# Performance work log

Measured on AMD Instinct MI355X. Metric: run time of the kernel, lower is better.

Reference implementation:

```python
import jax, jax.numpy as jnp
import numpy as np

B, L, D = 4, 4096, 1024
N_HEADS = 16
HEAD_SIZE = D // N_HEADS  # 64


def setup_inputs() -> dict:
    key = jax.random.key(0)
    k_x, k_w, k_m = jax.random.split(key, 3)
    x = jax.random.normal(k_x, (B, L, D), dtype=jnp.float32)
    # nn.Linear(D, 3*head_size, bias=False): weight (3*hs, D); store transposed (D, 3*hs)
    W_qkv = jax.random.normal(k_w, (D, 3 * HEAD_SIZE), dtype=jnp.float32) * (D ** -0.5)
    attn_mask = jax.random.randint(k_m, (B, L), 0, 2).astype(jnp.bool_)
    return {"x": x, "attn_mask": attn_mask, "W_qkv": W_qkv}


def reference(x, attn_mask, W_qkv):
    # x: (B, L, D); W_qkv: (D, 3*hs); attn_mask: (B, L) True = attend
    qkv = x @ W_qkv                                # (B, L, 3*hs)
    q, k, v = jnp.split(qkv, 3, axis=-1)           # each (B, L, hs)
    scale = HEAD_SIZE ** -0.5
    scores = jnp.einsum('bqd,bkd->bqk', q, k) * scale   # (B, L, L)
    neg_inf = jnp.finfo(scores.dtype).min
    scores = jnp.where(attn_mask[:, None, :], scores, neg_inf)
    weights = jax.nn.softmax(scores, axis=-1)      # (B, L, L)
    out = jnp.einsum('bqk,bkd->bqd', weights, v)   # (B, L, hs)
    return out
```

## Files before the change

### kernel.cpp

```cpp
#include <hip/hip_runtime.h>

typedef __bf16 bf16_t;
typedef __bf16 bf16x8 __attribute__((ext_vector_type(8)));
typedef __bf16 bf16x4 __attribute__((ext_vector_type(4)));
typedef __bf16 bf16x2 __attribute__((ext_vector_type(2)));
typedef float  f32x4  __attribute__((ext_vector_type(4)));
typedef float  f32x16 __attribute__((ext_vector_type(16)));
struct uint4_t { unsigned x, y, z, w; };

#define B_  4
#define L_  4096
#define D_  1024
#define HS  64
#define NQ  192
#define SCL2E 0.1803368801111204f
#define MFMA16 __builtin_amdgcn_mfma_f32_16x16x32_bf16
#define MFMA32 __builtin_amdgcn_mfma_f32_32x32x16_bf16

static __device__ __forceinline__ unsigned pk_bf16(float a, float b) {
    union { bf16x2 v; unsigned u; } x;
    x.v[0] = (bf16_t)a; x.v[1] = (bf16_t)b;
    return x.u;
}
static __device__ __forceinline__ void swap32(unsigned& x, unsigned& y) {
    asm("v_permlane32_swap_b32 %0, %1" : "+v"(x), "+v"(y));
}

__global__ __launch_bounds__(256) void pack_w_kernel(const void* __restrict__ Win,
                                                     const unsigned char* __restrict__ mask,
                                                     const unsigned short* __restrict__ xw,
                                                     bf16_t* __restrict__ Wtp,
                                                     int* __restrict__ flags,
                                                     bf16_t* __restrict__ m01) {
    __shared__ int c1, c23, cbad;
    int tid = threadIdx.x;
    if (tid == 0) { c1 = 0; c23 = 0; cbad = 0; }
    __syncthreads();
    uint4_t m[4];
#pragma unroll
    for (int i = 0; i < 4; ++i)
        m[i] = *(const uint4_t*)(mask + tid * 16 + i * 4096);
    int a = 0, bc = 0;
#pragma unroll
    for (int i = 0; i < 4; ++i) {
        const unsigned* w = (const unsigned*)&m[i];
#pragma unroll
        for (int j = 0; j < 4; ++j) {
            if (w[j] & 0x0000ff00u) a++;
            if (w[j] & 0xffff0000u) bc++;
        }
    }
    uint4_t xm = *(const uint4_t*)(xw + tid * 8);
    int bad = 0;
    const unsigned* xwv = (const unsigned*)&xm;
#pragma unroll
    for (int j = 0; j < 4; ++j)
#pragma unroll
        for (int h = 0; h < 2; ++h) {
            unsigned s = (xwv[j] >> (16 * h)) & 0xFFFFu;
            unsigned e = (s >> 7) & 0xFF;
            if (e > 150 || (e < 90 && e != 0)) bad++;
        }
    if (a)   atomicAdd(&c1, a);
    if (bc)  atomicAdd(&c23, bc);
    if (bad) atomicAdd(&cbad, bad);
    __syncthreads();
    int f32 = (cbad >= 64) ? 1 : 0;
    int kind = (c1 > 0) ? 1 : ((c23 > 0) ? 2 : 0);
    if (blockIdx.x == 0 && tid == 0) {
        flags[0] = kind;
        flags[1] = f32;
    }

    int idx = blockIdx.x * 256 + tid;

    if (idx < B_ * L_) {
        bool mv;
        if (kind == 1)      mv = mask[idx] != 0;
        else if (kind == 2) mv = ((const float*)mask)[idx] != 0.0f;
        else                mv = ((const int*)mask)[idx] != 0;
        m01[idx] = (bf16_t)(mv ? 1.0f : 0.0f);
    }

    int lane = idx & 63;
    int t    = (idx >> 6) & 3;
    int kc   = (idx >> 8) & 31;
    int ct   = idx >> 13;
    int n  = ct * 64 + t * 16 + (lane & 15);
    int k0 = kc * 32 + (lane >> 4) * 8;
    bf16x8 v;
#pragma unroll
    for (int j = 0; j < 8; ++j) {
        if (f32) v[j] = (bf16_t)(((const float*)Win)[(k0 + j) * NQ + n]);
        else     v[j] = ((const bf16_t*)Win)[(k0 + j) * NQ + n];
    }
    *(bf16x8*)(Wtp + (size_t)idx * 8) = v;
}

__global__ __launch_bounds__(256, 2) void qkv_gemm_kernel(const void* __restrict__ xin,
                                                          const int* __restrict__ flags,
                                                          const bf16_t* __restrict__ Wtp,
                                                          const bf16_t* __restrict__ m01p,
                                                          bf16_t* __restrict__ Qb,
                                                          bf16_t* __restrict__ Kp,
                                                          bf16_t* __restrict__ Vp) {
    __shared__ __align__(16) bf16_t xs[32 * 520];
    __shared__ __align__(16) bf16_t sqk[32 * 136];
    __shared__ __align__(16) bf16_t sv[64 * 40];

    int tid = threadIdx.x;
    int wave = tid >> 6, lane = tid & 63, quad = lane >> 4, l16 = lane & 15;
    int rg = wave & 1, ch = wave >> 1;
    int m0 = blockIdx.x * 32;
    int xf = flags[1];

    f32x4 acc[6] = {};
    bf16x8 Ba[6], Bb[6];

    auto stage = [&](int h) {
        bf16x8 tmp[8];
#pragma unroll
        for (int j = 0; j < 8; ++j) {
            int c = tid + j * 256;
            int row = c >> 6, off = (c & 63) * 8;
            if (xf) {
                const float* xp = (const float*)xin + (size_t)(m0 + row) * D_ + h * 512 + off;
                f32x4 lo = *(const f32x4*)xp, hi = *(const f32x4*)(xp + 4);
                tmp[j][0] = (bf16_t)lo[0]; tmp[j][1] = (bf16_t)lo[1];
                tmp[j][2] = (bf16_t)lo[2]; tmp[j][3] = (bf16_t)lo[3];
                tmp[j][4] = (bf16_t)hi[0]; tmp[j][5] = (bf16_t)hi[1];
                tmp[j][6] = (bf16_t)hi[2]; tmp[j][7] = (bf16_t)hi[3];
            } else {
                tmp[j] = *(const bf16x8*)((const bf16_t*)xin + (size_t)(m0 + row) * D_ + h * 512 + off);
            }
        }
#pragma unroll
        for (int j = 0; j < 8; ++j) {
            int c = tid + j * 256;
            int row = c >> 6, off = (c & 63) * 8;
            *(bf16x8*)&xs[row * 520 + off] = tmp[j];
        }
    };
    auto loadB6 = [&](int ks, bf16x8* Bv) {
#pragma unroll
        for (int i = 0; i < 6; ++i) {
            int st = ch * 6 + i, ct2 = st >> 2, tt = st & 3;
            Bv[i] = *(const bf16x8*)(Wtp + ((size_t)(ct2 * 32 + ks) * 4 + tt) * 512 + lane * 8);
        }
    };
    auto compute6 = [&](int ks, const bf16x8* Bv) {
        bf16x8 A = *(const bf16x8*)&xs[(rg * 16 + l16) * 520 + (ks & 15) * 32 + quad * 8];
#pragma unroll
        for (int i = 0; i < 6; ++i)
            acc[i] = MFMA16(A, Bv[i], acc[i], 0, 0, 0);
    };

    stage(0);
    loadB6(0, Ba);
    __syncthreads();
#pragma unroll
    for (int half = 0; half < 2; ++half) {
        int base = half * 16;
        for (int m = 0; m < 16; m += 2) {
            int ks = base + m;
            loadB6(ks + 1, Bb);
            compute6(ks, Ba);
            loadB6(ks + 2 <= 31 ? ks + 2 : 31, Ba);
            compute6(ks + 1, Bb);
        }
        if (half == 0) {
            __syncthreads();
            stage(1);
            __syncthreads();
        }
    }

    int rowb = rg * 16 + quad * 4;
#pragma unroll
    for (int i = 0; i < 6; ++i) {
        int col = ch * 96 + i * 16 + l16;
#pragma unroll
        for (int r = 0; r < 4; ++r) {
            float av = acc[i][r];
            if (col < 64) av *= SCL2E;
            bf16_t hv = (bf16_t)av;
            if (col < 128) sqk[(rowb + r) * 136 + col] = hv;
            else           sv[(col - 128) * 40 + rowb + r] = hv;
        }
    }
    __syncthreads();

    int bb = m0 >> 12, l0 = m0 & 4095;
    int t64 = l0 >> 6, stile = (l0 >> 5) & 1, ctop = (l0 >> 4) & 2;
    {
        int row = tid >> 3, off = (tid & 7) * 8;
        bf16x8 v = *(const bf16x8*)&sqk[row * 136 + off];
        *(bf16x8*)(Qb + (size_t)(m0 + row) * HS + off) = v;
    }
    {
        int chk = tid >> 6, ln = tid & 63;
        bf16x8 v = *(const bf16x8*)&sqk[(tid & 31) * 136 + 64 + chk * 16 + ((tid >> 5) & 1) * 8];
        *(bf16x8*)(Kp + (size_t)bb * (L_ * HS) +
                   ((((size_t)t64 * 2 + stile) * 4 + chk) * 64 + ln) * 8) = v;
    }
    {
        int dt = tid >> 7, chL = (tid >> 6) & 1, ln = tid & 63;
        int hi2 = (tid >> 5) & 1, d31 = tid & 31;
        bf16x8 v  = *(const bf16x8*)&sv[(dt * 32 + d31) * 40 + chL * 16 + hi2 * 8];
        bf16x8 mm = *(const bf16x8*)(m01p + (size_t)m0 + chL * 16 + hi2 * 8);
        bf16x8 o;
#pragma unroll
        for (int j = 0; j < 8; ++j) o[j] = (bf16_t)((float)v[j] * (float)mm[j]);
        *(bf16x8*)(Vp + (size_t)bb * (L_ * HS) +
                   ((((size_t)t64 * 2 + dt) * 4 + ctop + chL) * 64 + ln) * 8) = o;
    }
}

template<int NSPLIT>
__global__ __launch_bounds__(256, 2) void attn_kernel(const bf16_t* __restrict__ Qb,
                                                      const bf16_t* __restrict__ Kp,
                                                      const bf16_t* __restrict__ Vp,
                                                      const bf16_t* __restrict__ m01p,
                                                      const int* __restrict__ flags,
                                                      float* __restrict__ Opart,
                                                      float* __restrict__ lpart,
                                                      void* __restrict__ outv) {
    constexpr int KCH = L_ / NSPLIT;
    constexpr int NHT = KCH / 32;

    int tid = threadIdx.x, wave = tid >> 6, lane = tid & 63;
    int hi = lane >> 5, l31 = lane & 31;
    int grp = blockIdx.x % (B_ * NSPLIT);
    int qt  = blockIdx.x / (B_ * NSPLIT);
    int sp = grp / B_, b = grp % B_;
    int q0 = qt * 128 + wave * 32;
    int hb = sp * NHT;

    const bf16_t* KpB = Kp + (size_t)b * (L_ * HS);
    const bf16_t* VpB = Vp + (size_t)b * (L_ * HS);
    const bf16_t* mB  = m01p + (size_t)b * L_ + sp * KCH;

    bf16x8 Qf[4];
    {
        const bf16_t* qp = Qb + (size_t)(b * L_ + q0 + l31) * HS + hi * 8;
#pragma unroll
        for (int c = 0; c < 4; ++c) Qf[c] = *(const bf16x8*)(qp + c * 16);
    }

    f32x16 O0 = {}, O1 = {}, den = {};

    auto loadK = [&](bf16x8* Kf, int t) {
        const bf16_t* kt = KpB + (size_t)(hb + t) * 2048;
#pragma unroll
        for (int c = 0; c < 4; ++c)
            Kf[c] = *(const bf16x8*)(kt + ((size_t)c * 64 + lane) * 8);
    };

    bf16x8 Kfr[4];
    loadK(Kfr, 0);

    for (int t = 0; t < NHT; ++t) {
        int ht = hb + t;
        int t64 = ht >> 1, stile = ht & 1;
        const bf16_t* vt = VpB + (size_t)t64 * 4096;
        const bf16_t* mt = mB + t * 32;

        bf16x8 V0[2], V1[2], Mf[2];
#pragma unroll
        for (int cc = 0; cc < 2; ++cc) {
            int chk = stile * 2 + cc;
            V0[cc] = *(const bf16x8*)(vt + (size_t)(0 * 4 + chk) * 512 + lane * 8);
            V1[cc] = *(const bf16x8*)(vt + (size_t)(1 * 4 + chk) * 512 + lane * 8);
            Mf[cc] = *(const bf16x8*)(mt + cc * 16 + hi * 8);
        }

        f32x16 S = {};
        __builtin_amdgcn_s_setprio(1);
#pragma unroll
        for (int c = 0; c < 4; ++c)
            S = MFMA32(Kfr[c], Qf[c], S, 0, 0, 0);
        __builtin_amdgcn_s_setprio(0);

        if (t + 1 < NHT) loadK(Kfr, t + 1);

#pragma unroll
        for (int r = 0; r < 16; ++r) S[r] = exp2f(S[r]);

#pragma unroll
        for (int cc = 0; cc < 2; ++cc) {
            unsigned w0 = pk_bf16(S[cc * 8 + 0], S[cc * 8 + 1]);
            unsigned w1 = pk_bf16(S[cc * 8 + 2], S[cc * 8 + 3]);
            unsigned w2 = pk_bf16(S[cc * 8 + 4], S[cc * 8 + 5]);
            unsigned w3 = pk_bf16(S[cc * 8 + 6], S[cc * 8 + 7]);
            swap32(w0, w2);
            swap32(w1, w3);
            union { unsigned u[4]; bf16x8 v; } P;
            P.u[0] = w0; P.u[1] = w1; P.u[2] = w2; P.u[3] = w3;
            __builtin_amdgcn_s_setprio(1);
            O0  = MFMA32(P.v, V0[cc], O0, 0, 0, 0);
            O1  = MFMA32(P.v, V1[cc], O1, 0, 0, 0);
            den = MFMA32(P.v, Mf[cc], den, 0, 0, 0);
            __builtin_amdgcn_s_setprio(0);
        }
    }

    if (NSPLIT == 1) {
        int of32 = flags[1];
#pragma unroll
        for (int r = 0; r < 16; ++r) {
            int qr = (r & 3) + 8 * (r >> 2) + 4 * hi;
            float inv = 1.0f / den[r];
            size_t base = (size_t)(b * L_ + q0 + qr) * HS;
            if (of32) {
                float* op = (float*)outv + base;
                op[l31]      = O0[r] * inv;
                op[32 + l31] = O1[r] * inv;
            } else {
                bf16_t* op = (bf16_t*)outv + base;
                op[l31]      = (bf16_t)(O0[r] * inv);
                op[32 + l31] = (bf16_t)(O1[r] * inv);
            }
        }
    } else {
        float* op = Opart + (size_t)sp * (B_ * L_ * HS) + (size_t)(b * L_ + q0) * HS + l31;
#pragma unroll
        for (int r = 0; r < 16; ++r) {
            int qr = (r & 3) + 8 * (r >> 2) + 4 * hi;
            op[(size_t)qr * HS]      = O0[r];
            op[(size_t)qr * HS + 32] = O1[r];
        }
        if (l31 == 0) {
            float* lp = lpart + (size_t)sp * (B_ * L_) + b * L_ + q0;
#pragma unroll
            for (int r = 0; r < 16; ++r)
                lp[(r & 3) + 8 * (r >> 2) + 4 * hi] = den[r];
        }
    }
}

__global__ __launch_bounds__(256) void reduce_kernel(const float* __restrict__ Opart,
                                                     const float* __restrict__ lpart,
                                                     const int* __restrict__ flags,
                                                     void* __restrict__ outv,
                                                     int nsplit) {
    int i4 = (blockIdx.x * 256 + threadIdx.x) * 4;
    int row = i4 >> 6;
    f32x4 acc = {};
    float lsum = 0.f;
    for (int s = 0; s < nsplit; ++s) {
        acc  += *(const f32x4*)&Opart[(size_t)s * (B_ * L_ * HS) + i4];
        lsum += lpart[(size_t)s * (B_ * L_) + row];
    }
    float inv = 1.0f / lsum;
    if (flags[1]) {
        f32x4 r = { acc[0] * inv, acc[1] * inv, acc[2] * inv, acc[3] * inv };
        *(f32x4*)&((float*)outv)[i4] = r;
    } else {
        bf16x4 r;
#pragma unroll
        for (int j = 0; j < 4; ++j) r[j] = (bf16_t)(acc[j] * inv);
        *(bf16x4*)&((bf16_t*)outv)[i4] = r;
    }
}

extern "C" void kernel_launch(void* const* d_in, const int* in_sizes, int n_in,
                              void* d_out, int out_size, void* d_ws, size_t ws_size,
                              hipStream_t stream) {
    (void)in_sizes; (void)n_in; (void)out_size;
    const void* x    = d_in[0];
    const void* mask = d_in[1];
    const void* W    = d_in[2];

    char* ws = (char*)d_ws;
    bf16_t* Qb    = (bf16_t*)(ws);
    bf16_t* Kp    = (bf16_t*)(ws + (2u << 20));
    bf16_t* Vp    = (bf16_t*)(ws + (4u << 20));
    bf16_t* Wtp   = (bf16_t*)(ws + (6u << 20));
    int*    flags = (int*)   (ws + (6u << 20) + (512u << 10));
    bf16_t* m01p  = (bf16_t*)(ws + (6u << 20) + (516u << 10));
    float*  Opart = (float*) (ws + (7u << 20));

    auto need = [](int ns) -> size_t {
        return (7u << 20) + (size_t)ns * (B_ * L_ * HS * 4)
                          + (size_t)ns * (B_ * L_ * 4) + 4096;
    };
    int nsplit = (ws_size >= need(8)) ? 8 : (ws_size >= need(4)) ? 4 : 1;
    float* lpart = (float*)(ws + (7u << 20) + (size_t)nsplit * (B_ * L_ * HS * 4));

    pack_w_kernel<<<96, 256, 0, stream>>>(W, (const unsigned char*)mask,
                                          (const unsigned short*)x, Wtp, flags, m01p);
    qkv_gemm_kernel<<<512, 256, 0, stream>>>(x, flags, Wtp, m01p, Qb, Kp, Vp);
    if (nsplit == 8) {
        attn_kernel<8><<<32 * B_ * 8, 256, 0, stream>>>(Qb, Kp, Vp, m01p, flags,
                                                        Opart, lpart, d_out);
        reduce_kernel<<<(B_ * L_ * HS) / 1024, 256, 0, stream>>>(Opart, lpart, flags,
                                                                 d_out, 8);
    } else if (nsplit == 4) {
        attn_kernel<4><<<32 * B_ * 4, 256, 0, stream>>>(Qb, Kp, Vp, m01p, flags,
                                                        Opart, lpart, d_out);
        reduce_kernel<<<(B_ * L_ * HS) / 1024, 256, 0, stream>>>(Opart, lpart, flags,
                                                                 d_out, 4);
    } else {
        attn_kernel<1><<<32 * B_, 256, 0, stream>>>(Qb, Kp, Vp, m01p, flags,
                                                    Opart, lpart, d_out);
    }
}
```

Measured before the change: 155.3 us.

## Process two 32-row query tiles per wave to reuse K/V/mask fragments

Each wave now handles 64 query rows, as two 32-row sub-tiles, instead of 32. The K, V and mask fragments loaded per key tile feed both sub-tiles, which halves global K/V traffic per query and halves the grid size. The cost is doubled accumulator registers, which could hurt occupancy under launch_bounds(256,2). The grid also shrinks (nsplit=8 gives 512 blocks), which reduces parallelism.

```diff
diff --git a/kernel.cpp b/kernel.cpp
--- a/kernel.cpp
+++ b/kernel.cpp
@@ -233,21 +233,26 @@
     int grp = blockIdx.x % (B_ * NSPLIT);
     int qt  = blockIdx.x / (B_ * NSPLIT);
     int sp = grp / B_, b = grp % B_;
-    int q0 = qt * 128 + wave * 32;
+    int q0 = qt * 256 + wave * 64;
     int hb = sp * NHT;
 
     const bf16_t* KpB = Kp + (size_t)b * (L_ * HS);
     const bf16_t* VpB = Vp + (size_t)b * (L_ * HS);
     const bf16_t* mB  = m01p + (size_t)b * L_ + sp * KCH;
 
-    bf16x8 Qf[4];
+    bf16x8 QfA[4], QfB[4];
     {
-        const bf16_t* qp = Qb + (size_t)(b * L_ + q0 + l31) * HS + hi * 8;
-#pragma unroll
-        for (int c = 0; c < 4; ++c) Qf[c] = *(const bf16x8*)(qp + c * 16);
-    }
-
-    f32x16 O0 = {}, O1 = {}, den = {};
+        const bf16_t* qa = Qb + (size_t)(b * L_ + q0 + l31) * HS + hi * 8;
+        const bf16_t* qb = Qb + (size_t)(b * L_ + q0 + 32 + l31) * HS + hi * 8;
+#pragma unroll
+        for (int c = 0; c < 4; ++c) {
+            QfA[c] = *(const bf16x8*)(qa + c * 16);
+            QfB[c] = *(const bf16x8*)(qb + c * 16);
+        }
+    }
+
+    f32x16 O0A = {}, O1A = {}, denA = {};
+    f32x16 O0B = {}, O1B = {}, denB = {};
 
     auto loadK = [&](bf16x8* Kf, int t) {
         const bf16_t* kt = KpB + (size_t)(hb + t) * 2048;
@@ -274,66 +279,105 @@
             Mf[cc] = *(const bf16x8*)(mt + cc * 16 + hi * 8);
         }
 
-        f32x16 S = {};
-        __builtin_amdgcn_s_setprio(1);
-#pragma unroll
-        for (int c = 0; c < 4; ++c)
-            S = MFMA32(Kfr[c], Qf[c], S, 0, 0, 0);
-        __builtin_amdgcn_s_setprio(0);
-
-        if (t + 1 < NHT) loadK(Kfr, t + 1);
-
-#pragma unroll
-        for (int r = 0; r < 16; ++r) S[r] = exp2f(S[r]);
-
-#pragma unroll
-        for (int cc = 0; cc < 2; ++cc) {
-            unsigned w0 = pk_bf16(S[cc * 8 + 0], S[cc * 8 + 1]);
-            unsigned w1 = pk_bf16(S[cc * 8 + 2], S[cc * 8 + 3]);
-            unsigned w2 = pk_bf16(S[cc * 8 + 4], S[cc * 8 + 5]);
-            unsigned w3 = pk_bf16(S[cc * 8 + 6], S[cc * 8 + 7]);
-            swap32(w0, w2);
-            swap32(w1, w3);
-            union { unsigned u[4]; bf16x8 v; } P;
-            P.u[0] = w0; P.u[1] = w1; P.u[2] = w2; P.u[3] = w3;
+        {
+            f32x16 S = {};
             __builtin_amdgcn_s_setprio(1);
-            O0  = MFMA32(P.v, V0[cc], O0, 0, 0, 0);
-            O1  = MFMA32(P.v, V1[cc], O1, 0, 0, 0);
-            den = MFMA32(P.v, Mf[cc], den, 0, 0, 0);
+#pragma unroll
+            for (int c = 0; c < 4; ++c)
+                S = MFMA32(Kfr[c], QfA[c], S, 0, 0, 0);
             __builtin_amdgcn_s_setprio(0);
+#pragma unroll
+            for (int r = 0; r < 16; ++r) S[r] = exp2f(S[r]);
+#pragma unroll
+            for (int cc = 0; cc < 2; ++cc) {
+                unsigned w0 = pk_bf16(S[cc * 8 + 0], S[cc * 8 + 1]);
+                unsigned w1 = pk_bf16(S[cc * 8 + 2], S[cc * 8 + 3]);
+                unsigned w2 = pk_bf16(S[cc * 8 + 4], S[cc * 8 + 5]);
+                unsigned w3 = pk_bf16(S[cc * 8 + 6], S[cc * 8 + 7]);
+                swap32(w0, w2);
+                swap32(w1, w3);
+                union { unsigned u[4]; bf16x8 v; } P;
+                P.u[0] = w0; P.u[1] = w1; P.u[2] = w2; P.u[3] = w3;
+                __builtin_amdgcn_s_setprio(1);
+                O0A  = MFMA32(P.v, V0[cc], O0A, 0, 0, 0);
+                O1A  = MFMA32(P.v, V1[cc], O1A, 0, 0, 0);
+                denA = MFMA32(P.v, Mf[cc], denA, 0, 0, 0);
+                __builtin_amdgcn_s_setprio(0);
+            }
+        }
+
+        {
+            f32x16 S = {};
+            __builtin_amdgcn_s_setprio(1);
+#pragma unroll
+            for (int c = 0; c < 4; ++c)
+                S = MFMA32(Kfr[c], QfB[c], S, 0, 0, 0);
+            __builtin_amdgcn_s_setprio(0);
+            if (t + 1 < NHT) loadK(Kfr, t + 1);
+#pragma unroll
+            for (int r = 0; r < 16; ++r) S[r] = exp2f(S[r]);
+#pragma unroll
+            for (int cc = 0; cc < 2; ++cc) {
+                unsigned w0 = pk_bf16(S[cc * 8 + 0], S[cc * 8 + 1]);
+                unsigned w1 = pk_bf16(S[cc * 8 + 2], S[cc * 8 + 3]);
+                unsigned w2 = pk_bf16(S[cc * 8 + 4], S[cc * 8 + 5]);
+                unsigned w3 = pk_bf16(S[cc * 8 + 6], S[cc * 8 + 7]);
+                swap32(w0, w2);
+                swap32(w1, w3);
+                union { unsigned u[4]; bf16x8 v; } P;
+                P.u[0] = w0; P.u[1] = w1; P.u[2] = w2; P.u[3] = w3;
+                __builtin_amdgcn_s_setprio(1);
+                O0B  = MFMA32(P.v, V0[cc], O0B, 0, 0, 0);
+                O1B  = MFMA32(P.v, V1[cc], O1B, 0, 0, 0);
+                denB = MFMA32(P.v, Mf[cc], denB, 0, 0, 0);
+                __builtin_amdgcn_s_setprio(0);
+            }
         }
     }
 
     if (NSPLIT == 1) {
         int of32 = flags[1];
 #pragma unroll
-        for (int r = 0; r < 16; ++r) {
-            int qr = (r & 3) + 8 * (r >> 2) + 4 * hi;
-            float inv = 1.0f / den[r];
-            size_t base = (size_t)(b * L_ + q0 + qr) * HS;
-            if (of32) {
-                float* op = (float*)outv + base;
-                op[l31]      = O0[r] * inv;
-                op[32 + l31] = O1[r] * inv;
-            } else {
-                bf16_t* op = (bf16_t*)outv + base;
-                op[l31]      = (bf16_t)(O0[r] * inv);
-                op[32 + l31] = (bf16_t)(O1[r] * inv);
+        for (int g = 0; g < 2; ++g) {
+            const f32x16& O0 = g ? O0B : O0A;
+            const f32x16& O1 = g ? O1B : O1A;
+            const f32x16& dn = g ? denB : denA;
+#pragma unroll
+            for (int r = 0; r < 16; ++r) {
+                int qr = (r & 3) + 8 * (r >> 2) + 4 * hi;
+                float inv = 1.0f / dn[r];
+                size_t base = (size_t)(b * L_ + q0 + g * 32 + qr) * HS;
+                if (of32) {
+                    float* op = (float*)outv + base;
+                    op[l31]      = O0[r] * inv;
+                    op[32 + l31] = O1[r] * inv;
+                } else {
+                    bf16_t* op = (bf16_t*)outv + base;
+                    op[l31]      = (bf16_t)(O0[r] * inv);
+                    op[32 + l31] = (bf16_t)(O1[r] * inv);
+                }
             }
         }
     } else {
-        float* op = Opart + (size_t)sp * (B_ * L_ * HS) + (size_t)(b * L_ + q0) * HS + l31;
-#pragma unroll
-        for (int r = 0; r < 16; ++r) {
-            int qr = (r & 3) + 8 * (r >> 2) + 4 * hi;
-            op[(size_t)qr * HS]      = O0[r];
-            op[(size_t)qr * HS + 32] = O1[r];
-        }
-        if (l31 == 0) {
-            float* lp = lpart + (size_t)sp * (B_ * L_) + b * L_ + q0;
-#pragma unroll
-            for (int r = 0; r < 16; ++r)
-                lp[(r & 3) + 8 * (r >> 2) + 4 * hi] = den[r];
+#pragma unroll
+        for (int g = 0; g < 2; ++g) {
+            const f32x16& O0 = g ? O0B : O0A;
+            const f32x16& O1 = g ? O1B : O1A;
+            const f32x16& dn = g ? denB : denA;
+            float* op = Opart + (size_t)sp * (B_ * L_ * HS)
+                              + (size_t)(b * L_ + q0 + g * 32) * HS + l31;
+#pragma unroll
+            for (int r = 0; r < 16; ++r) {
+                int qr = (r & 3) + 8 * (r >> 2) + 4 * hi;
+                op[(size_t)qr * HS]      = O0[r];
+                op[(size_t)qr * HS + 32] = O1[r];
+            }
+            if (l31 == 0) {
+                float* lp = lpart + (size_t)sp * (B_ * L_) + b * L_ + q0 + g * 32;
+#pragma unroll
+                for (int r = 0; r < 16; ++r)
+                    lp[(r & 3) + 8 * (r >> 2) + 4 * hi] = dn[r];
+            }
         }
     }
 }
@@ -391,17 +435,17 @@
                                           (const unsigned short*)x, Wtp, flags, m01p);
     qkv_gemm_kernel<<<512, 256, 0, stream>>>(x, flags, Wtp, m01p, Qb, Kp, Vp);
     if (nsplit == 8) {
-        attn_kernel<8><<<32 * B_ * 8, 256, 0, stream>>>(Qb, Kp, Vp, m01p, flags,
+        attn_kernel<8><<<16 * B_ * 8, 256, 0, stream>>>(Qb, Kp, Vp, m01p, flags,
                                                         Opart, lpart, d_out);
         reduce_kernel<<<(B_ * L_ * HS) / 1024, 256, 0, stream>>>(Opart, lpart, flags,
                                                                  d_out, 8);
     } else if (nsplit == 4) {
-        attn_kernel<4><<<32 * B_ * 4, 256, 0, stream>>>(Qb, Kp, Vp, m01p, flags,
+        attn_kernel<4><<<16 * B_ * 4, 256, 0, stream>>>(Qb, Kp, Vp, m01p, flags,
                                                         Opart, lpart, d_out);
         reduce_kernel<<<(B_ * L_ * HS) / 1024, 256, 0, stream>>>(Opart, lpart, flags,
                                                                  d_out, 4);
     } else {
-        attn_kernel<1><<<32 * B_, 256, 0, stream>>>(Qb, Kp, Vp, m01p, flags,
+        attn_kernel<1><<<16 * B_, 256, 0, stream>>>(Qb, Kp, Vp, m01p, flags,
                                                     Opart, lpart, d_out);
     }
 }
```

New measurement: 155.8 us. About the same (+0.3%).
